# Optimization experiments

Measured on AMD Instinct MI355X. Metric: run time of the kernel, lower is better.

The kernel has to match this reference:

```python
import jax, jax.numpy as jnp
import numpy as np


def _conv(x, w, b):
    # NCHW conv, SAME padding for odd kernel, stride 1
    pad = (w.shape[2] - 1) // 2
    y = jax.lax.conv_general_dilated(
        x, w, window_strides=(1, 1), padding=[(pad, pad), (pad, pad)],
        dimension_numbers=('NCHW', 'OIHW', 'NCHW'))
    return y + b[None, :, None, None]


def _cell(x, h, c, m, p):
    # one TransGRU cell step; x:[B,Cin,H,W], h/c/m:[B,hc,H,W]
    A = _conv(jnp.concatenate([x, h], axis=1), p['w_rzo'], p['b_rzo'])   # [B,3hc,H,W]
    Bm = _conv(jnp.concatenate([x, m], axis=1), p['w_rz'], p['b_rz'])    # [B,2hc,H,W]
    decay_h = jnp.exp(-p['td_h'])[None]          # (1,hc,1,1)
    decay_m = jnp.exp(-p['td_m'])[None]
    gate = jax.nn.sigmoid(p['tg'])[None]
    Ar, Az, Ao = jnp.split(A, 3, axis=1)
    Br, Bz = jnp.split(Bm, 2, axis=1)
    r = jax.nn.sigmoid(Ar * gate + h * decay_h)
    z = jax.nn.sigmoid(Az * gate + h * decay_h)
    o = jax.nn.sigmoid(Ao)
    xr = jax.nn.sigmoid(Br * gate + m * decay_m)
    xz = jax.nn.sigmoid(Bz * gate + m * decay_m)
    gc = jnp.tanh(_conv(jnp.concatenate([x, r * c], axis=1), p['w_h'], p['b_h']))
    gm = jnp.tanh(_conv(jnp.concatenate([x, xr * m], axis=1), p['w_h'], p['b_h']))
    c_new = z * c + (1 - z) * gc
    m_new = xz * m + (1 - xz) * gm
    h_new = o * jnp.tanh(_conv(jnp.concatenate([c_new, m_new], axis=1), p['w_o'], p['b_o']))
    return h_new, c_new, m_new, (r, z, xr, xz, c_new, m_new, gc, gm, o)


def _forward(x, params, attention_size):
    B, T, _, H, W = x.shape
    L = len(params)
    hcs = [p['w_rzo'].shape[0] // 3 for p in params]
    hc_last = hcs[-1]
    dtype = x.dtype
    init_states = tuple(
        tuple(jnp.zeros((B, hc, H, W), dtype) for _ in range(3)) for hc in hcs)
    init_gates = tuple(jnp.zeros((B, hc_last, H, W), dtype) for _ in range(9))

    def step(carry, xt):
        states, _ = carry
        inp = xt
        m = states[-1][2]  # layer 0 reads m from last layer of previous step
        new_states = []
        gates = None
        for l in range(L):
            h, c, _own_m = states[l]
            inp, cn, mn, gates = _cell(inp, h, c, m, params[l])
            new_states.append((inp, cn, mn))
            m = mn  # next layer reads m just produced by this layer
        return (tuple(new_states), gates), inp

    (final_states, gates), hs = jax.lax.scan(
        step, (init_states, init_gates), jnp.swapaxes(x, 0, 1))
    # gates from last layer at final step (matches torch leaking loop vars)
    r, z, xr, xz, c, m, gc, gm, o = gates
    q = ((r + xr + c + gc) * 0.25).reshape(B, hc_last, H * W)
    k = ((r + xr + m + gm) * 0.25).reshape(B, hc_last, H * W)
    v = jnp.swapaxes(hs, 0, 1).reshape(B, T, hc_last, H * W)
    scale = 1.0 / float(np.sqrt(attention_size))
    attn = jax.nn.softmax(jnp.einsum('bcn,bdn->bcd', q, k) * scale, axis=-1)
    out = jnp.einsum('bcd,btdn->btcn', attn, v).reshape(B, T, hc_last, H, W)
    return out


def setup_inputs() -> dict:
    key = jax.random.key(0)
    ks = jax.random.split(key, 32)
    d = {'x': jax.random.normal(ks[0], (4, 8, 16, 64, 64), jnp.float32)}
    specs = {
        'w_rzo0': (192, 80, 3, 3), 'b_rzo0': (192,), 'w_rz0': (128, 80, 3, 3),
        'b_rz0': (128,), 'w_h0': (64, 80, 3, 3), 'b_h0': (64,),
        'w_o0': (64, 128, 1, 1), 'b_o0': (64,), 'td_h0': (64, 1, 1),
        'td_m0': (64, 1, 1), 'tg0': (64, 1, 1),
        'w_rzo1': (192, 128, 3, 3), 'b_rzo1': (192,), 'w_rz1': (128, 128, 3, 3),
        'b_rz1': (128,), 'w_h1': (64, 128, 3, 3), 'b_h1': (64,),
        'w_o1': (64, 128, 1, 1), 'b_o1': (64,), 'td_h1': (64, 1, 1),
        'td_m1': (64, 1, 1), 'tg1': (64, 1, 1),
    }
    for i, (name, shp) in enumerate(specs.items()):
        d[name] = jax.random.normal(ks[i + 1], shp, jnp.float32) * 0.05
    d['attention_size'] = 4096
    return d


def reference(x, w_rzo0, b_rzo0, w_rz0, b_rz0, w_h0, b_h0, w_o0, b_o0,
              td_h0, td_m0, tg0, w_rzo1, b_rzo1, w_rz1, b_rz1, w_h1, b_h1,
              w_o1, b_o1, td_h1, td_m1, tg1, attention_size):
    params = [
        dict(w_rzo=w_rzo0, b_rzo=b_rzo0, w_rz=w_rz0, b_rz=b_rz0, w_h=w_h0,
             b_h=b_h0, w_o=w_o0, b_o=b_o0, td_h=td_h0, td_m=td_m0, tg=tg0),
        dict(w_rzo=w_rzo1, b_rzo=b_rzo1, w_rz=w_rz1, b_rz=b_rz1, w_h=w_h1,
             b_h=b_h1, w_o=w_o1, b_o=b_o1, td_h=td_h1, td_m=td_m1, tg=tg1),
    ]
    return _forward(x, params, attention_size)
```

## Files before the change

### kernel.cpp

```cpp
#include <hip/hip_runtime.h>
#include <math.h>

#define HWN 4096
#define Bn 4
#define Tn 8

typedef __attribute__((ext_vector_type(8))) _Float16 f16x8;
typedef __attribute__((ext_vector_type(4))) float floatx4;

__device__ __forceinline__ float fexp2_(float x) { return __builtin_amdgcn_exp2f(x); }
__device__ __forceinline__ float frcp_(float x)  { return __builtin_amdgcn_rcpf(x); }
__device__ __forceinline__ float sigmoidf_(float v) {
    return frcp_(1.f + fexp2_(v * -1.44269504089f));
}
__device__ __forceinline__ float tanhf_(float v) {
    float vc = fminf(fmaxf(v, -15.f), 15.f);
    float t = fexp2_(vc * 2.88539008178f);
    return (t - 1.f) * frcp_(t + 1.f);
}

__device__ __forceinline__ void split8(const float* vv, f16x8* hi, f16x8* lo) {
#pragma unroll
    for (int j = 0; j < 8; ++j) {
        _Float16 h = (_Float16)vv[j];
        (*hi)[j] = h;
        (*lo)[j] = (_Float16)(vv[j] - (float)h);
    }
}

struct PW  { const float* W; _Float16* dst; int Ctot, Cout, nch, KK; };
struct PW8 { PW p[8]; };

__global__ __launch_bounds__(256) void prep_w_all(PW8 d)
{
    const PW e = d.p[blockIdx.y];
    const int ncog = e.Cout >> 4;
    const long total = (long)e.KK * e.nch * ncog * 512;
    for (long i = (long)blockIdx.x * 256 + threadIdx.x; i < total;
         i += (long)gridDim.x * 256) {
        int j    = (int)(i & 7);
        int lane = (int)((i >> 3) & 63);
        long r   = i >> 9;
        int f = (int)(r % ncog); r /= ncog;
        int c = (int)(r % e.nch);  r /= e.nch;
        int kk = (int)r;
        int co = f * 16 + (lane & 15);
        int ci = c * 32 + (lane >> 4) * 8 + j;
        float v = (ci < e.Ctot) ? e.W[((long)co * e.Ctot + ci) * e.KK + kk] : 0.f;
        _Float16 hi = (_Float16)v;
        e.dst[i]         = hi;
        e.dst[total + i] = (_Float16)(v - (float)hi);
    }
}

__global__ __launch_bounds__(256) void prep_x_kernel(
    const float* __restrict__ x, float* __restrict__ xcl)
{
    const int i = blockIdx.x * 256 + threadIdx.x;
    const int px = i & 4095;
    const int t  = (i >> 12) & 7;
    const int b  = i >> 15;
    float* d = xcl + (((long)t * Bn + b) * HWN + px) * 16;
#pragma unroll
    for (int ch = 0; ch < 16; ++ch)
        d[ch] = x[((long)(b * 8 + t) * 16 + ch) * HWN + px];
}

__global__ void prep_gc2(const float* __restrict__ tg0, const float* __restrict__ tdh0,
                         const float* __restrict__ tdm0, float* __restrict__ gc0,
                         const float* __restrict__ tg1, const float* __restrict__ tdh1,
                         const float* __restrict__ tdm1, float* __restrict__ gc1)
{
    const int j = threadIdx.x;
    const float* tg  = blockIdx.x ? tg1  : tg0;
    const float* tdh = blockIdx.x ? tdh1 : tdh0;
    const float* tdm = blockIdx.x ? tdm1 : tdm0;
    float* gc        = blockIdx.x ? gc1  : gc0;
    gc[j]       = 1.f / (1.f + expf(-tg[j]));
    gc[64 + j]  = expf(-tdh[j]);
    gc[128 + j] = expf(-tdm[j]);
}

template<int EPI, int NF, int TR>
__global__ __launch_bounds__(256) void conv3m(
    const float* __restrict__ in1, int C1,
    const float* __restrict__ in2a, const float* __restrict__ in2b,
    int Ctot, int nch,
    const _Float16* __restrict__ wA, const float* __restrict__ biasA,
    float* outA, int CoutA, int ncogA,
    const _Float16* __restrict__ wB, const float* __restrict__ biasB,
    float* outB, int CoutB, int ncogB, int nA,
    float* s1, float* s2, float* s3, float* s4,
    float* s5, float* s6, float* s7, float* s8,
    const float* __restrict__ gc, int last)
{
    constexpr int G = TR / 4;
    constexpr int SLOTS = (TR + 2) * 18 * 4;
    constexpr int NS = (SLOTS + 255) / 256;
    __shared__ __align__(16) _Float16 ldsB[TR + 2][18][2][40];

    const int tid = threadIdx.x;
    const int ty0 = (blockIdx.x >> 2) * TR;
    const int tx0 = (blockIdx.x & 3) * 16;
    const int b   = blockIdx.z & 3;
    const int which = (EPI == 1) ? (int)(blockIdx.z >> 2)
                                 : (blockIdx.y >= (unsigned)nA ? 1 : 0);

    const float*    in2  = which ? in2b : in2a;
    const _Float16* Wf   = which ? wB : wA;
    const float*    bias = which ? biasB : biasA;
    float*          outp = which ? outB : outA;
    const int Cout = which ? CoutB : CoutA;
    const int ncog = which ? ncogB : ncogA;
    const int cog0 = (EPI == 1) ? blockIdx.y * NF
                   : (which ? (blockIdx.y - nA) * NF : blockIdx.y * NF);
    const int co0  = cog0 * 16;

    const int lane = tid & 63, wv = tid >> 6, tl = lane & 15, quad = lane >> 4;
    const int C2 = Ctot - C1;
    const long wplane = (long)9 * nch * ncog * 512;
    const float* in1b  = in1 + (long)b * HWN * C1;
    const float* in2bb = in2 + (long)b * HWN * C2;

    floatx4 acc[NF][G];
#pragma unroll
    for (int f = 0; f < NF; ++f)
#pragma unroll
        for (int g = 0; g < G; ++g) acc[f][g] = (floatx4){0.f, 0.f, 0.f, 0.f};

    float4 pa[NS], pb[NS];
    auto prefetch = [&](int c) {
        const int c0 = c * 32;
#pragma unroll
        for (int s = 0; s < NS; ++s) {
            const int i = tid + s * 256;
            float4 va = {0.f, 0.f, 0.f, 0.f}, vb = {0.f, 0.f, 0.f, 0.f};
            if (i < SLOTS) {
                const int pxh = i >> 2, cig = i & 3;
                const int yh = pxh / 18, xh = pxh - yh * 18;
                const int y = ty0 + yh - 1, x = tx0 + xh - 1;
                const int ch = c0 + cig * 8;
                if (ch < Ctot && (unsigned)y < 64u && (unsigned)x < 64u) {
                    const float* src; long off;
                    if (ch < C1) { src = in1b;  off = (long)(y * 64 + x) * C1 + ch; }
                    else         { src = in2bb; off = (long)(y * 64 + x) * C2 + ch - C1; }
                    va = *(const float4*)(src + off);
                    vb = *(const float4*)(src + off + 4);
                }
            }
            pa[s] = va; pb[s] = vb;
        }
    };

    prefetch(0);

    for (int c = 0; c < nch; ++c) {
        f16x8 wh[5][NF], wl[5][NF];
#define LOADW(S, BUF)                                                           \
        {                                                                       \
            const int kk_ = ((S) % 3) * 3 + (S) / 3;                            \
            const long wo_ = ((long)(kk_ * nch + c) * ncog + cog0) * 512 + lane * 8; \
            _Pragma("unroll")                                                   \
            for (int f = 0; f < NF; ++f) {                                      \
                wh[BUF][f] = *(const f16x8*)(Wf + wo_ + (long)f * 512);         \
                wl[BUF][f] = *(const f16x8*)(Wf + wplane + wo_ + (long)f * 512);\
            }                                                                   \
        }
        LOADW(0, 0)
        LOADW(1, 1)
        LOADW(2, 2)
        LOADW(3, 3)

        __syncthreads();
#pragma unroll
        for (int s = 0; s < NS; ++s) {
            const int i = tid + s * 256;
            if (i < SLOTS) {
                const int pxh = i >> 2, cig = i & 3;
                const int yh = pxh / 18, xh = pxh - yh * 18;
                float vv[8] = {pa[s].x, pa[s].y, pa[s].z, pa[s].w,
                               pb[s].x, pb[s].y, pb[s].z, pb[s].w};
                f16x8 vh, vl;
                split8(vv, &vh, &vl);
                *(f16x8*)&ldsB[yh][xh][0][cig * 8] = vh;
                *(f16x8*)&ldsB[yh][xh][1][cig * 8] = vl;
            }
        }
        __syncthreads();

#pragma unroll
        for (int kx = 0; kx < 3; ++kx) {
            f16x8 rh[G + 2], rl[G + 2];
#pragma unroll
            for (int rr = 0; rr < G + 2; ++rr) {
                const _Float16* pB = &ldsB[wv * G + rr][tl + kx][0][quad * 8];
                rh[rr] = *(const f16x8*)pB;
                rl[rr] = *(const f16x8*)(pB + 40);
            }
#pragma unroll
            for (int ky = 0; ky < 3; ++ky) {
                const int s = kx * 3 + ky;
                if (s < 5) LOADW(s + 4, (s + 4) % 5)
                const int cur = s % 5;
#pragma unroll
                for (int f = 0; f < NF; ++f)
#pragma unroll
                    for (int g = 0; g < G; ++g) {
                        acc[f][g] = __builtin_amdgcn_mfma_f32_16x16x32_f16(wh[cur][f], rh[g + ky], acc[f][g], 0, 0, 0);
                        acc[f][g] = __builtin_amdgcn_mfma_f32_16x16x32_f16(wh[cur][f], rl[g + ky], acc[f][g], 0, 0, 0);
                        acc[f][g] = __builtin_amdgcn_mfma_f32_16x16x32_f16(wl[cur][f], rh[g + ky], acc[f][g], 0, 0, 0);
                    }
            }
            if (kx == 1 && c + 1 < nch) prefetch(c + 1);
        }
#undef LOADW
    }

    if (EPI == 0) {
        const int gid = co0 >> 6;
        const long bb64 = (long)b * HWN * 64;
        const float* dec = which ? in2b : in2a;
        const float* cs  = (const float*)s8;
        float* g0   = which ? s2 : s1;
        float* g1   = which ? s4 : s3;
        float* rout = which ? s7 : s6;
#pragma unroll
        for (int f = 0; f < NF; ++f) {
            const int co = co0 + f * 16 + quad * 4;
            const int ch = co & 63;
            float gvc[4], dvc[4];
            if (gid < 2) {
#pragma unroll
                for (int j = 0; j < 4; ++j) {
                    gvc[j] = gc[ch + j];
                    dvc[j] = gc[(which ? 128 : 64) + ch + j];
                }
            }
#pragma unroll
            for (int g = 0; g < G; ++g) {
                const long px = (long)(ty0 + wv * G + g) * 64 + tx0 + tl;
                const long off = bb64 + px * 64 + ch;
                float vv[4];
                vv[0] = acc[f][g][0] + bias[co + 0];
                vv[1] = acc[f][g][1] + bias[co + 1];
                vv[2] = acc[f][g][2] + bias[co + 2];
                vv[3] = acc[f][g][3] + bias[co + 3];
                if (gid == 2) {
                    float ov[4];
#pragma unroll
                    for (int j = 0; j < 4; ++j) ov[j] = sigmoidf_(vv[j]);
                    *(float4*)(s5 + off) = *(float4*)ov;
                } else {
                    float4 dv = *(const float4*)(dec + off);
                    const float* dvp = (const float*)&dv;
                    float rr[4];
#pragma unroll
                    for (int j = 0; j < 4; ++j)
                        rr[j] = sigmoidf_(vv[j] * gvc[j] + dvp[j] * dvc[j]);
                    if (gid == 0) {
                        float4 sv = dv;
                        if (!which) sv = *(const float4*)(cs + off);
                        const float* svp = (const float*)&sv;
                        float outv[4];
#pragma unroll
                        for (int j = 0; j < 4; ++j) outv[j] = rr[j] * svp[j];
                        *(float4*)(g0 + off) = *(float4*)outv;
                        if (last) *(float4*)(rout + off) = *(float4*)rr;
                    } else {
                        *(float4*)(g1 + off) = *(float4*)rr;
                    }
                }
            }
        }
    } else {
        const float* zt = which ? s2 : s1;
        const float* st = which ? s4 : s3;
        float* qk = which ? s8 : s7;
#pragma unroll
        for (int f = 0; f < NF; ++f) {
            const int co = co0 + f * 16 + quad * 4;
#pragma unroll
            for (int g = 0; g < G; ++g) {
                const long px = (long)(ty0 + wv * G + g) * 64 + tx0 + tl;
                const long off = (long)b * HWN * 64 + px * 64 + co;
                float4 zv = *(const float4*)(zt + off);
                float4 sv = *(const float4*)(st + off);
                float gv[4], cn[4];
                gv[0] = tanhf_(acc[f][g][0] + bias[co + 0]);
                gv[1] = tanhf_(acc[f][g][1] + bias[co + 1]);
                gv[2] = tanhf_(acc[f][g][2] + bias[co + 2]);
                gv[3] = tanhf_(acc[f][g][3] + bias[co + 3]);
                cn[0] = zv.x * sv.x + (1.f - zv.x) * gv[0];
                cn[1] = zv.y * sv.y + (1.f - zv.y) * gv[1];
                cn[2] = zv.z * sv.z + (1.f - zv.z) * gv[2];
                cn[3] = zv.w * sv.w + (1.f - zv.w) * gv[3];
                *(float4*)(outp + off) = *(float4*)cn;
                if (last) {
                    float4 rv = *(const float4*)(s5 + off);
                    float4 xv = *(const float4*)(s6 + off);
                    qk[((long)(b * 64) + co + 0) * HWN + px] = 0.25f * (rv.x + xv.x + cn[0] + gv[0]);
                    qk[((long)(b * 64) + co + 1) * HWN + px] = 0.25f * (rv.y + xv.y + cn[1] + gv[1]);
                    qk[((long)(b * 64) + co + 2) * HWN + px] = 0.25f * (rv.z + xv.z + cn[2] + gv[2]);
                    qk[((long)(b * 64) + co + 3) * HWN + px] = 0.25f * (rv.w + xv.w + cn[3] + gv[3]);
                }
            }
        }
    }
}

__global__ __launch_bounds__(256) void conv1x1m(
    const float* __restrict__ cten, const float* __restrict__ mten,
    const float* __restrict__ oten,
    const _Float16* __restrict__ W, const float* __restrict__ bias,
    float* houtp)
{
    const int tid = threadIdx.x;
    const int lane = tid & 63, wv = tid >> 6, tl = lane & 15, quad = lane >> 4;
    const int b = blockIdx.y;
    const int fh = blockIdx.x & 1;
    const int px = (blockIdx.x >> 1) * 64 + wv * 16 + tl;
    const long bb = (long)b * HWN * 64;

    f16x8 wh[4][2], wl[4][2];
#pragma unroll
    for (int c = 0; c < 4; ++c)
#pragma unroll
        for (int f = 0; f < 2; ++f) {
            const long wo = (long)(c * 4 + fh * 2 + f) * 512 + lane * 8;
            wh[c][f] = *(const f16x8*)(W + wo);
            wl[c][f] = *(const f16x8*)(W + 8192 + wo);
        }
    f16x8 bh[4], bl[4];
#pragma unroll
    for (int c = 0; c < 4; ++c) {
        const float* src = (c < 2) ? cten : mten;
        const int ch0 = (c & 1) * 32 + quad * 8;
        const long off = bb + (long)px * 64 + ch0;
        float4 p0 = *(const float4*)(src + off);
        float4 p1 = *(const float4*)(src + off + 4);
        float vv[8] = {p0.x, p0.y, p0.z, p0.w, p1.x, p1.y, p1.z, p1.w};
        split8(vv, &bh[c], &bl[c]);
    }

    floatx4 acc[2];
#pragma unroll
    for (int f = 0; f < 2; ++f) acc[f] = (floatx4){0.f, 0.f, 0.f, 0.f};
#pragma unroll
    for (int c = 0; c < 4; ++c)
#pragma unroll
        for (int f = 0; f < 2; ++f) {
            acc[f] = __builtin_amdgcn_mfma_f32_16x16x32_f16(wh[c][f], bh[c], acc[f], 0, 0, 0);
            acc[f] = __builtin_amdgcn_mfma_f32_16x16x32_f16(wh[c][f], bl[c], acc[f], 0, 0, 0);
            acc[f] = __builtin_amdgcn_mfma_f32_16x16x32_f16(wl[c][f], bh[c], acc[f], 0, 0, 0);
        }

#pragma unroll
    for (int f = 0; f < 2; ++f) {
        const int co = fh * 32 + f * 16 + quad * 4;
        const long off = bb + (long)px * 64 + co;
        float4 ov = *(const float4*)(oten + off);
        float4 hv;
        hv.x = ov.x * tanhf_(acc[f][0] + bias[co + 0]);
        hv.y = ov.y * tanhf_(acc[f][1] + bias[co + 1]);
        hv.z = ov.z * tanhf_(acc[f][2] + bias[co + 2]);
        hv.w = ov.w * tanhf_(acc[f][3] + bias[co + 3]);
        *(float4*)(houtp + off) = hv;
    }
}

__global__ __launch_bounds__(256) void logits_part(
    const float* __restrict__ q, const float* __restrict__ k, float* __restrict__ part)
{
    __shared__ float qs[64][66], ks[64][66];
    const int tid = threadIdx.x;
    const int b = blockIdx.x, kc = blockIdx.y;
    const int cqq = tid >> 4, ckq = tid & 15;
    float pacc[4][4];
#pragma unroll
    for (int u = 0; u < 4; ++u)
#pragma unroll
        for (int v = 0; v < 4; ++v) pacc[u][v] = 0.f;

    for (int sub = 0; sub < 4; ++sub) {
        const int px0 = kc * 256 + sub * 64;
        __syncthreads();
#pragma unroll
        for (int rr = 0; rr < 16; ++rr) {
            const int idx = rr * 256 + tid;
            const int chh = idx >> 6, pxo = idx & 63;
            qs[chh][pxo] = q[((long)b * 64 + chh) * HWN + px0 + pxo];
            ks[chh][pxo] = k[((long)b * 64 + chh) * HWN + px0 + pxo];
        }
        __syncthreads();
        for (int p = 0; p < 64; ++p) {
            float qv[4], kv[4];
#pragma unroll
            for (int u = 0; u < 4; ++u) { qv[u] = qs[cqq + 16 * u][p]; kv[u] = ks[ckq + 16 * u][p]; }
#pragma unroll
            for (int u = 0; u < 4; ++u)
#pragma unroll
                for (int v = 0; v < 4; ++v) pacc[u][v] = fmaf(qv[u], kv[v], pacc[u][v]);
        }
    }
#pragma unroll
    for (int u = 0; u < 4; ++u)
#pragma unroll
        for (int v = 0; v < 4; ++v)
            part[(((long)b * 16 + kc) * 64 + cqq + 16 * u) * 64 + ckq + 16 * v] = pacc[u][v];
}

__global__ void reduce_softmax(const float* __restrict__ part, float* __restrict__ attn)
{
    const int row = blockIdx.x;
    const int b = row >> 6, cq = row & 63;
    const int lane = threadIdx.x;
    float s = 0.f;
#pragma unroll
    for (int kc = 0; kc < 16; ++kc)
        s += part[(((long)b * 16 + kc) * 64 + cq) * 64 + lane];
    float v = s * (1.f / 64.f);
    float mx = v;
    for (int off = 32; off; off >>= 1) mx = fmaxf(mx, __shfl_xor(mx, off));
    float e = fexp2_((v - mx) * 1.44269504089f);
    float sum = e;
    for (int off = 32; off; off >>= 1) sum += __shfl_xor(sum, off);
    attn[row * 64 + lane] = e / sum;
}

__global__ __launch_bounds__(256) void out_cl(
    const float* __restrict__ attn, const float* __restrict__ hs,
    float* __restrict__ outp)
{
    __shared__ __align__(16) float att_t[64][8];
    const int bt = blockIdx.x;
    const int b = bt >> 3, t = bt & 7;
    const int c0 = blockIdx.z * 8;
    const int tid = threadIdx.x;
    for (int i = tid; i < 512; i += 256) {
        int d = i >> 3, j = i & 7;
        att_t[d][j] = attn[(b * 64 + c0 + j) * 64 + d];
    }
    __syncthreads();

    const long px = blockIdx.y * 256 + tid;
    const long SLOT = (long)Bn * HWN * 64;
    const float* vb = hs + (long)t * SLOT + ((long)b * HWN + px) * 64;

    float acc[8];
#pragma unroll
    for (int j = 0; j < 8; ++j) acc[j] = 0.f;
#pragma unroll 4
    for (int dg = 0; dg < 16; ++dg) {
        float4 v4 = *(const float4*)(vb + dg * 4);
        const float* vp = (const float*)&v4;
#pragma unroll
        for (int j4 = 0; j4 < 4; ++j4) {
            const float vv = vp[j4];
            const float4 a0 = *(const float4*)&att_t[dg * 4 + j4][0];
            const float4 a1 = *(const float4*)&att_t[dg * 4 + j4][4];
            acc[0] = fmaf(vv, a0.x, acc[0]); acc[1] = fmaf(vv, a0.y, acc[1]);
            acc[2] = fmaf(vv, a0.z, acc[2]); acc[3] = fmaf(vv, a0.w, acc[3]);
            acc[4] = fmaf(vv, a1.x, acc[4]); acc[5] = fmaf(vv, a1.y, acc[5]);
            acc[6] = fmaf(vv, a1.z, acc[6]); acc[7] = fmaf(vv, a1.w, acc[7]);
        }
    }
    const long ob = ((long)(b * 8 + t) * 64 + c0) * HWN + px;
#pragma unroll
    for (int j = 0; j < 8; ++j) outp[ob + (long)j * HWN] = acc[j];
}

extern "C" void kernel_launch(void* const* d_in, const int* in_sizes, int n_in,
                              void* d_out, int out_size, void* d_ws, size_t ws_size,
                              hipStream_t stream)
{
    const float* x = (const float*)d_in[0];
    const float* w_rzo[2] = {(const float*)d_in[1],  (const float*)d_in[12]};
    const float* b_rzo[2] = {(const float*)d_in[2],  (const float*)d_in[13]};
    const float* w_rz[2]  = {(const float*)d_in[3],  (const float*)d_in[14]};
    const float* b_rz[2]  = {(const float*)d_in[4],  (const float*)d_in[15]};
    const float* w_h[2]   = {(const float*)d_in[5],  (const float*)d_in[16]};
    const float* b_h[2]   = {(const float*)d_in[6],  (const float*)d_in[17]};
    const float* w_o[2]   = {(const float*)d_in[7],  (const float*)d_in[18]};
    const float* b_o[2]   = {(const float*)d_in[8],  (const float*)d_in[19]};
    const float* td_h[2]  = {(const float*)d_in[9],  (const float*)d_in[20]};
    const float* td_m[2]  = {(const float*)d_in[10], (const float*)d_in[21]};
    const float* tg[2]    = {(const float*)d_in[11], (const float*)d_in[22]};

    const size_t S64 = (size_t)Bn * HWN * 64;
    float* P = (float*)d_ws;
    float* h0    = P; P += S64;
    float* c0    = P; P += S64;
    float* m0    = P; P += S64;
    float* c1    = P; P += S64;
    float* m1    = P; P += S64;
    float* zslab = P; P += S64;
    float* A_cl  = P; P += (size_t)Bn * HWN * 192;
    float* B_cl  = P; P += (size_t)Bn * HWN * 128;
    float* rb    = P; P += S64;
    float* xrb   = P; P += S64;
    float* zb    = P; P += S64;
    float* xzb   = P; P += S64;
    float* ogb   = P; P += S64;
    float* rcb   = P; P += S64;
    float* xmb   = P; P += S64;
    float* hs    = P; P += (size_t)Tn * S64;
    float* x_cl  = P; P += (size_t)Tn * Bn * HWN * 16;
    _Float16* wA0 = (_Float16*)P;
    _Float16* wB0 = wA0 + 331776;
    _Float16* wH0 = wB0 + 221184;
    _Float16* wA1 = wH0 + 110592;
    _Float16* wB1 = wA1 + 442368;
    _Float16* wH1 = wB1 + 294912;
    _Float16* wO0 = wH1 + 147456;
    _Float16* wO1 = wO0 + 16384;
    float* qbuf  = A_cl;
    float* kbuf  = qbuf + S64;
    float* partb = kbuf + S64;
    float* attnb = partb + (size_t)Bn * 16 * 64 * 64;
    float* gc0   = B_cl;
    float* gc1   = B_cl + 192;

    hipMemsetAsync(h0, 0, 6 * S64 * sizeof(float), stream);

    prep_x_kernel<<<512, 256, 0, stream>>>(x, x_cl);
    prep_gc2<<<2, 64, 0, stream>>>(tg[0], td_h[0], td_m[0], gc0,
                                   tg[1], td_h[1], td_m[1], gc1);
    PW8 pw;
    pw.p[0] = {w_rzo[0], wA0, 80, 192, 3, 9};
    pw.p[1] = {w_rz[0],  wB0, 80, 128, 3, 9};
    pw.p[2] = {w_h[0],   wH0, 80,  64, 3, 9};
    pw.p[3] = {w_rzo[1], wA1, 128, 192, 4, 9};
    pw.p[4] = {w_rz[1],  wB1, 128, 128, 4, 9};
    pw.p[5] = {w_h[1],   wH1, 128, 64, 4, 9};
    pw.p[6] = {w_o[0],   wO0, 128, 64, 4, 1};
    pw.p[7] = {w_o[1],   wO1, 128, 64, 4, 1};
    prep_w_all<<<dim3(128, 8), 256, 0, stream>>>(pw);

    for (int t = 0; t < Tn; ++t) {
        const float* xt = x_cl + (size_t)t * Bn * HWN * 16;
        const float* h1prev = (t == 0) ? zslab : (hs + (size_t)(t - 1) * S64);
        float* h1out = hs + (size_t)t * S64;
        const int lastq = (t == Tn - 1) ? 1 : 0;

        conv3m<0, 2, 16><<<dim3(16, 10, 4), 256, 0, stream>>>(
            xt, 16, h0, m1, 80, 3,
            wA0, b_rzo[0], nullptr, 192, 12,
            wB0, b_rz[0],  nullptr, 128, 8, 6,
            rcb, xmb, zb, xzb, ogb, rb, xrb, c0,
            gc0, 0);
        conv3m<1, 1, 8><<<dim3(32, 4, 8), 256, 0, stream>>>(
            xt, 16, rcb, xmb, 80, 3,
            wH0, b_h[0], c0, 64, 4,
            wH0, b_h[0], m0, 64, 4, 0,
            zb, xzb, c0, m1, rb, xrb, qbuf, kbuf,
            nullptr, 0);
        conv1x1m<<<dim3(128, 4), 256, 0, stream>>>(c0, m0, ogb, wO0, b_o[0], h0);

        conv3m<0, 2, 16><<<dim3(16, 10, 4), 256, 0, stream>>>(
            h0, 64, h1prev, m0, 128, 4,
            wA1, b_rzo[1], nullptr, 192, 12,
            wB1, b_rz[1],  nullptr, 128, 8, 6,
            rcb, xmb, zb, xzb, ogb, rb, xrb, c1,
            gc1, lastq);
        conv3m<1, 1, 8><<<dim3(32, 4, 8), 256, 0, stream>>>(
            h0, 64, rcb, xmb, 128, 4,
            wH1, b_h[1], c1, 64, 4,
            wH1, b_h[1], m1, 64, 4, 0,
            zb, xzb, c1, m0, rb, xrb, qbuf, kbuf,
            nullptr, lastq);
        conv1x1m<<<dim3(128, 4), 256, 0, stream>>>(c1, m1, ogb, wO1, b_o[1], h1out);
    }

    logits_part<<<dim3(4, 16), 256, 0, stream>>>(qbuf, kbuf, partb);
    reduce_softmax<<<256, 64, 0, stream>>>(partb, attnb);
    out_cl<<<dim3(32, 16, 8), 256, 0, stream>>>(attnb, hs, (float*)d_out);
}
```

Baseline: 1.192 ms.

## Double-buffer LDS input tiles in gate conv and halve its row tile

Adds a template parameter that gives the 3x3 conv kernel two LDS input buffers. While the current channel chunk is being multiplied, the next chunk is staged into the other buffer and its first weights are loaded, which drops one barrier per chunk. The gate-conv launches also switch from 16-row to 8-row tiles, doubling the grid to raise occupancy. The cost is more LDS and registers per block, and the smaller tile reuses each weight across fewer rows.

New measurement: 1.204 ms. Within noise of the previous version (+1.0%).

```diff
diff --git a/kernel.cpp b/kernel.cpp
--- a/kernel.cpp
+++ b/kernel.cpp
@@ -81,7 +81,7 @@
     gc[128 + j] = expf(-tdm[j]);
 }
 
-template<int EPI, int NF, int TR>
+template<int EPI, int NF, int TR, int DB>
 __global__ __launch_bounds__(256) void conv3m(
     const float* __restrict__ in1, int C1,
     const float* __restrict__ in2a, const float* __restrict__ in2b,
@@ -97,7 +97,7 @@
     constexpr int G = TR / 4;
     constexpr int SLOTS = (TR + 2) * 18 * 4;
     constexpr int NS = (SLOTS + 255) / 256;
-    __shared__ __align__(16) _Float16 ldsB[TR + 2][18][2][40];
+    __shared__ __align__(16) _Float16 ldsB[DB][TR + 2][18][2][40];
 
     const int tid = threadIdx.x;
     const int ty0 = (blockIdx.x >> 2) * TR;
@@ -151,27 +151,7 @@
             pa[s] = va; pb[s] = vb;
         }
     };
-
-    prefetch(0);
-
-    for (int c = 0; c < nch; ++c) {
-        f16x8 wh[5][NF], wl[5][NF];
-#define LOADW(S, BUF)                                                           \
-        {                                                                       \
-            const int kk_ = ((S) % 3) * 3 + (S) / 3;                            \
-            const long wo_ = ((long)(kk_ * nch + c) * ncog + cog0) * 512 + lane * 8; \
-            _Pragma("unroll")                                                   \
-            for (int f = 0; f < NF; ++f) {                                      \
-                wh[BUF][f] = *(const f16x8*)(Wf + wo_ + (long)f * 512);         \
-                wl[BUF][f] = *(const f16x8*)(Wf + wplane + wo_ + (long)f * 512);\
-            }                                                                   \
-        }
-        LOADW(0, 0)
-        LOADW(1, 1)
-        LOADW(2, 2)
-        LOADW(3, 3)
-
-        __syncthreads();
+    auto stage = [&](int buf) {
 #pragma unroll
         for (int s = 0; s < NS; ++s) {
             const int i = tid + s * 256;
@@ -182,39 +162,101 @@
                                pb[s].x, pb[s].y, pb[s].z, pb[s].w};
                 f16x8 vh, vl;
                 split8(vv, &vh, &vl);
-                *(f16x8*)&ldsB[yh][xh][0][cig * 8] = vh;
-                *(f16x8*)&ldsB[yh][xh][1][cig * 8] = vl;
+                *(f16x8*)&ldsB[buf][yh][xh][0][cig * 8] = vh;
+                *(f16x8*)&ldsB[buf][yh][xh][1][cig * 8] = vl;
             }
         }
+    };
+
+#define LOADWC(S, BUF, CC)                                                      \
+        {                                                                       \
+            const int kk_ = ((S) % 3) * 3 + (S) / 3;                            \
+            const long wo_ = ((long)(kk_ * nch + (CC)) * ncog + cog0) * 512 + lane * 8; \
+            _Pragma("unroll")                                                   \
+            for (int f = 0; f < NF; ++f) {                                      \
+                wh[BUF][f] = *(const f16x8*)(Wf + wo_ + (long)f * 512);         \
+                wl[BUF][f] = *(const f16x8*)(Wf + wplane + wo_ + (long)f * 512);\
+            }                                                                   \
+        }
+
+    prefetch(0);
+
+    if constexpr (DB == 2) {
+        f16x8 wh[5][NF], wl[5][NF];
+        LOADWC(0, 0, 0) LOADWC(1, 1, 0) LOADWC(2, 2, 0) LOADWC(3, 3, 0)
+        stage(0);
         __syncthreads();
-
-#pragma unroll
-        for (int kx = 0; kx < 3; ++kx) {
-            f16x8 rh[G + 2], rl[G + 2];
-#pragma unroll
-            for (int rr = 0; rr < G + 2; ++rr) {
-                const _Float16* pB = &ldsB[wv * G + rr][tl + kx][0][quad * 8];
-                rh[rr] = *(const f16x8*)pB;
-                rl[rr] = *(const f16x8*)(pB + 40);
+        if (1 < nch) prefetch(1);
+
+        for (int c = 0; c < nch; ++c) {
+            const int cur = c & 1;
+            const int more = (c + 1 < nch);
+#pragma unroll
+            for (int kx = 0; kx < 3; ++kx) {
+                f16x8 rh[G + 2], rl[G + 2];
+#pragma unroll
+                for (int rr = 0; rr < G + 2; ++rr) {
+                    const _Float16* pB = &ldsB[cur][wv * G + rr][tl + kx][0][quad * 8];
+                    rh[rr] = *(const f16x8*)pB;
+                    rl[rr] = *(const f16x8*)(pB + 40);
+                }
+                if (kx == 0 && more) stage(cur ^ 1);
+                if (kx == 1 && c + 2 < nch) prefetch(c + 2);
+#pragma unroll
+                for (int ky = 0; ky < 3; ++ky) {
+                    const int s = kx * 3 + ky;
+                    if (s < 5) LOADWC(s + 4, (s + 4) % 5, c)
+                    const int curw = s % 5;
+#pragma unroll
+                    for (int f = 0; f < NF; ++f)
+#pragma unroll
+                        for (int g = 0; g < G; ++g) {
+                            acc[f][g] = __builtin_amdgcn_mfma_f32_16x16x32_f16(wh[curw][f], rh[g + ky], acc[f][g], 0, 0, 0);
+                            acc[f][g] = __builtin_amdgcn_mfma_f32_16x16x32_f16(wh[curw][f], rl[g + ky], acc[f][g], 0, 0, 0);
+                            acc[f][g] = __builtin_amdgcn_mfma_f32_16x16x32_f16(wl[curw][f], rh[g + ky], acc[f][g], 0, 0, 0);
+                        }
+                    if (s >= 5 && more) LOADWC(s - 5, s - 5, c + 1)
+                }
             }
-#pragma unroll
-            for (int ky = 0; ky < 3; ++ky) {
-                const int s = kx * 3 + ky;
-                if (s < 5) LOADW(s + 4, (s + 4) % 5)
-                const int cur = s % 5;
-#pragma unroll
-                for (int f = 0; f < NF; ++f)
-#pragma unroll
-                    for (int g = 0; g < G; ++g) {
-                        acc[f][g] = __builtin_amdgcn_mfma_f32_16x16x32_f16(wh[cur][f], rh[g + ky], acc[f][g], 0, 0, 0);
-                        acc[f][g] = __builtin_amdgcn_mfma_f32_16x16x32_f16(wh[cur][f], rl[g + ky], acc[f][g], 0, 0, 0);
-                        acc[f][g] = __builtin_amdgcn_mfma_f32_16x16x32_f16(wl[cur][f], rh[g + ky], acc[f][g], 0, 0, 0);
-                    }
+            if (more) __syncthreads();
+        }
+    } else {
+        for (int c = 0; c < nch; ++c) {
+            f16x8 wh[5][NF], wl[5][NF];
+            LOADWC(0, 0, c) LOADWC(1, 1, c) LOADWC(2, 2, c) LOADWC(3, 3, c)
+
+            __syncthreads();
+            stage(0);
+            __syncthreads();
+
+#pragma unroll
+            for (int kx = 0; kx < 3; ++kx) {
+                f16x8 rh[G + 2], rl[G + 2];
+#pragma unroll
+                for (int rr = 0; rr < G + 2; ++rr) {
+                    const _Float16* pB = &ldsB[0][wv * G + rr][tl + kx][0][quad * 8];
+                    rh[rr] = *(const f16x8*)pB;
+                    rl[rr] = *(const f16x8*)(pB + 40);
+                }
+#pragma unroll
+                for (int ky = 0; ky < 3; ++ky) {
+                    const int s = kx * 3 + ky;
+                    if (s < 5) LOADWC(s + 4, (s + 4) % 5, c)
+                    const int curw = s % 5;
+#pragma unroll
+                    for (int f = 0; f < NF; ++f)
+#pragma unroll
+                        for (int g = 0; g < G; ++g) {
+                            acc[f][g] = __builtin_amdgcn_mfma_f32_16x16x32_f16(wh[curw][f], rh[g + ky], acc[f][g], 0, 0, 0);
+                            acc[f][g] = __builtin_amdgcn_mfma_f32_16x16x32_f16(wh[curw][f], rl[g + ky], acc[f][g], 0, 0, 0);
+                            acc[f][g] = __builtin_amdgcn_mfma_f32_16x16x32_f16(wl[curw][f], rh[g + ky], acc[f][g], 0, 0, 0);
+                        }
+                }
+                if (kx == 1 && c + 1 < nch) prefetch(c + 1);
             }
-            if (kx == 1 && c + 1 < nch) prefetch(c + 1);
-        }
-#undef LOADW
-    }
+        }
+    }
+#undef LOADWC
 
     if (EPI == 0) {
         const int gid = co0 >> 6;
@@ -542,13 +584,13 @@
         float* h1out = hs + (size_t)t * S64;
         const int lastq = (t == Tn - 1) ? 1 : 0;
 
-        conv3m<0, 2, 16><<<dim3(16, 10, 4), 256, 0, stream>>>(
+        conv3m<0, 2, 8, 2><<<dim3(32, 10, 4), 256, 0, stream>>>(
             xt, 16, h0, m1, 80, 3,
             wA0, b_rzo[0], nullptr, 192, 12,
             wB0, b_rz[0],  nullptr, 128, 8, 6,
             rcb, xmb, zb, xzb, ogb, rb, xrb, c0,
             gc0, 0);
-        conv3m<1, 1, 8><<<dim3(32, 4, 8), 256, 0, stream>>>(
+        conv3m<1, 1, 8, 1><<<dim3(32, 4, 8), 256, 0, stream>>>(
             xt, 16, rcb, xmb, 80, 3,
             wH0, b_h[0], c0, 64, 4,
             wH0, b_h[0], m0, 64, 4, 0,
@@ -556,13 +598,13 @@
             nullptr, 0);
         conv1x1m<<<dim3(128, 4), 256, 0, stream>>>(c0, m0, ogb, wO0, b_o[0], h0);
 
-        conv3m<0, 2, 16><<<dim3(16, 10, 4), 256, 0, stream>>>(
+        conv3m<0, 2, 8, 2><<<dim3(32, 10, 4), 256, 0, stream>>>(
             h0, 64, h1prev, m0, 128, 4,
             wA1, b_rzo[1], nullptr, 192, 12,
             wB1, b_rz[1],  nullptr, 128, 8, 6,
             rcb, xmb, zb, xzb, ogb, rb, xrb, c1,
             gc1, lastq);
-        conv3m<1, 1, 8><<<dim3(32, 4, 8), 256, 0, stream>>>(
+        conv3m<1, 1, 8, 1><<<dim3(32, 4, 8), 256, 0, stream>>>(
             h0, 64, rcb, xmb, 128, 4,
             wH1, b_h[1], c1, 64, 4,
             wH1, b_h[1], m1, 64, 4, 0,
```
